# Kernel tuning notes

Measured on AMD Instinct MI355X. Metric: run time of the kernel, lower is better.

## Reference

```python
import jax, jax.numpy as jnp
import numpy as np

T, B, IN_DIM, H = 512, 256, 512, 256  # H == hidden_dim == n_qubits

def setup_inputs() -> dict:
    key = jax.random.key(0)
    ks = jax.random.split(key, 13)
    inputs = jax.random.normal(ks[0], (T, B, IN_DIM), dtype=jnp.float32)
    d = IN_DIM + H
    s = 1.0 / np.sqrt(d)
    def lin(k):
        k1, k2 = jax.random.split(k)
        return (jax.random.uniform(k1, (H, d), jnp.float32, -s, s),
                jax.random.uniform(k2, (H,), jnp.float32, -s, s))
    Wf, bf = lin(ks[1]); Wi, bi = lin(ks[2]); Wg, bg = lin(ks[3]); Wo, bo = lin(ks[4])
    thf = jax.random.uniform(ks[5], (H,), jnp.float32)
    thi = jax.random.uniform(ks[6], (H,), jnp.float32)
    thg = jax.random.uniform(ks[7], (H,), jnp.float32)
    tho = jax.random.uniform(ks[8], (H,), jnp.float32)
    return dict(inputs=inputs, Wf=Wf, bf=bf, thf=thf, Wi=Wi, bi=bi, thi=thi,
                Wg=Wg, bg=bg, thg=thg, Wo=Wo, bo=bo, tho=tho)

def _qgate(combined, W, b, th):
    # Analytic form of the RY+RY+CNOT-ladder circuit with PauliZ expvals:
    # <Z_k> = prod_{i<=k} cos(z_i + theta_i), z = Linear(combined)
    z = combined @ W.T + b  # [B, H]
    return jnp.cumprod(jnp.cos(z + th), axis=-1)

def reference(inputs, Wf, bf, thf, Wi, bi, thi, Wg, bg, thg, Wo, bo, tho):
    batch = inputs.shape[1]
    hx0 = jnp.zeros((batch, H), inputs.dtype)
    cx0 = jnp.zeros((batch, H), inputs.dtype)

    def step(carry, x):
        hx, cx = carry
        comb = jnp.concatenate([x, hx], axis=1)  # [B, IN_DIM+H]
        f = jax.nn.sigmoid(_qgate(comb, Wf, bf, thf))
        i = jax.nn.sigmoid(_qgate(comb, Wi, bi, thi))
        g = jnp.tanh(_qgate(comb, Wg, bg, thg))
        o = jax.nn.sigmoid(_qgate(comb, Wo, bo, tho))
        cx = f * cx + i * g
        hx = o * jnp.tanh(cx)
        return (hx, cx), hx

    (hx, cx), stacked = jax.lax.scan(step, (hx0, cx0), inputs)
    return stacked, hx, cx
```

## Files before the change

kernel.cpp:

```cpp
#include <hip/hip_runtime.h>
#include <hip/hip_bf16.h>
#include <stdint.h>

#define T_STEPS 512
#define BATCH   256
#define HID     256

#define NRWG   128
#define NWWG   128
#define NWG    256
#define RING   4
#define CHUNK  8
#define NCHUNK 64
#define TPC    64
#define SLOT_F (CHUNK*256*1024)

using short8 = __attribute__((ext_vector_type(8))) short;
using f32x4  = __attribute__((ext_vector_type(4))) float;

#define VMCNT0() asm volatile("s_waitcnt vmcnt(0)" ::: "memory")

__device__ inline unsigned short f2bf(float f) {
  unsigned u = __float_as_uint(f);
  unsigned r = (u + 0x7fffu + ((u >> 16) & 1u)) >> 16;
  return (unsigned short)r;
}
__device__ inline float sigm(float x)   { return __builtin_amdgcn_rcpf(1.0f + __expf(-x)); }
__device__ inline float tanh_f(float x) { return 2.0f * __builtin_amdgcn_rcpf(1.0f + __expf(-2.0f * x)) - 1.0f; }

__device__ inline int ld_rlx(const int* p) {
  return __hip_atomic_load(p, __ATOMIC_RELAXED, __HIP_MEMORY_SCOPE_AGENT);
}
__device__ inline void st_rlx(int* p, int v) {
  __hip_atomic_store(p, v, __ATOMIC_RELAXED, __HIP_MEMORY_SCOPE_AGENT);
}
__device__ inline void add_rlx(int* p, int v) {
  __hip_atomic_fetch_add(p, v, __ATOMIC_RELAXED, __HIP_MEMORY_SCOPE_AGENT);
}
__device__ inline float ldg_coh(const float* p) {
  return __hip_atomic_load(p, __ATOMIC_RELAXED, __HIP_MEMORY_SCOPE_AGENT);
}
__device__ inline void stg_coh(float* p, float v) {
  __hip_atomic_store(p, v, __ATOMIC_RELAXED, __HIP_MEMORY_SCOPE_AGENT);
}

__global__ __launch_bounds__(256) void prep_kernel(
    const float* __restrict__ Wf, const float* __restrict__ Wi,
    const float* __restrict__ Wg, const float* __restrict__ Wo,
    const float* __restrict__ bf_, const float* __restrict__ bi_,
    const float* __restrict__ bg_, const float* __restrict__ bo_,
    const float* __restrict__ thf, const float* __restrict__ thi,
    const float* __restrict__ thg, const float* __restrict__ tho,
    unsigned short* __restrict__ Wfull, float* __restrict__ cvec,
    int* __restrict__ flags)
{
  int j = blockIdx.x;
  int g = j >> 8, col = j & 255;
  const float* W  = (g==0)?Wf:(g==1)?Wi:(g==2)?Wg:Wo;
  const float* bb = (g==0)?bf_:(g==1)?bi_:(g==2)?bg_:bo_;
  const float* th = (g==0)?thf:(g==1)?thi:(g==2)?thg:tho;
  const float* wrow = W + (size_t)col * 768;
  for (int k = threadIdx.x; k < 768; k += blockDim.x)
    Wfull[(size_t)j * 768 + k] = f2bf(wrow[k]);
  if (threadIdx.x == 0) cvec[j] = bb[col] + th[col];
  if (j == 0) for (int i = threadIdx.x; i < 512; i += 256) flags[i] = 0;
}

__global__ __launch_bounds__(512, 2) void persist_kernel(
    const float* __restrict__ X,
    const unsigned short* __restrict__ Wfull,
    const float* __restrict__ cvec,
    float* __restrict__ ring,
    float* __restrict__ exch,
    int* __restrict__ done,
    int* __restrict__ consumed,
    int* __restrict__ seq,
    float* __restrict__ out)
{
  __shared__ union {
    struct { unsigned short h[16][264]; float z[8][264]; } rec;
    struct { unsigned short a[128][40]; unsigned short b[256][40]; } gem;
  } sm;

  int bid = blockIdx.x, tid = threadIdx.x;
  int lane = tid & 63, wv = tid >> 6;
  int l15 = lane & 15, lk = lane >> 4;

  if (bid < NRWG) {
    int bg = bid >> 2, g = bid & 3;

    for (int i = tid; i < 16*264; i += 512) ((unsigned short*)sm.rec.h)[i] = 0;

    short8 af[2][8];
#pragma unroll
    for (int ti = 0; ti < 2; ++ti)
#pragma unroll
      for (int kk = 0; kk < 8; ++kk)
        af[ti][kk] = *(const short8*)(Wfull +
            (size_t)(g*256 + wv*32 + ti*16 + l15)*768 + 512 + kk*32 + lk*8);

    float creg[4] = {0.f, 0.f, 0.f, 0.f};
    float zx[4];
    __syncthreads();

    for (int t = 0; t < T_STEPS; ++t) {
      int cIdx = t >> 3;
      if ((t & 7) == 0) {
        if (tid == 0) { while (ld_rlx(&done[cIdx]) < TPC) __builtin_amdgcn_s_sleep(1); }
        __syncthreads();
        const float* zp = ring + (size_t)(cIdx & (RING-1))*SLOT_F
                        + ((size_t)(t & 7)*256 + bg*8 + wv)*1024 + g*256 + lane;
#pragma unroll
        for (int s = 0; s < 4; ++s) zx[s] = ldg_coh(zp + s*64);
      }

      short8 bfr[8];
#pragma unroll
      for (int kk = 0; kk < 8; ++kk)
        bfr[kk] = *(const short8*)&sm.rec.h[l15][kk*32 + lk*8];
      f32x4 acc0 = {0.f,0.f,0.f,0.f}, acc1 = {0.f,0.f,0.f,0.f};
#pragma unroll
      for (int kk = 0; kk < 8; ++kk) {
        acc0 = __builtin_amdgcn_mfma_f32_16x16x32_bf16(af[0][kk], bfr[kk], acc0, 0, 0, 0);
        acc1 = __builtin_amdgcn_mfma_f32_16x16x32_bf16(af[1][kk], bfr[kk], acc1, 0, 0, 0);
      }
      if (l15 < 8) {
        *(f32x4*)&sm.rec.z[l15][wv*32 +      lk*4] = acc0;
        *(f32x4*)&sm.rec.z[l15][wv*32 + 16 + lk*4] = acc1;
      }
      __syncthreads();

      float v[4];
#pragma unroll
      for (int s = 0; s < 4; ++s)
        v[s] = __cosf(sm.rec.z[wv][s*64 + lane] + zx[s]);
#pragma unroll
      for (int off = 1; off < 64; off <<= 1) {
        float u0 = __shfl_up(v[0], (unsigned)off, 64);
        float u1 = __shfl_up(v[1], (unsigned)off, 64);
        float u2 = __shfl_up(v[2], (unsigned)off, 64);
        float u3 = __shfl_up(v[3], (unsigned)off, 64);
        if (lane >= off) { v[0]*=u0; v[1]*=u1; v[2]*=u2; v[3]*=u3; }
      }
      float t0 = __shfl(v[0], 63, 64), t1 = __shfl(v[1], 63, 64), t2 = __shfl(v[2], 63, 64);
      float p1 = t0, p2 = t0*t1, p3 = p2*t2;
      float a0 = v[0], a1 = v[1]*p1, a2 = v[2]*p2, a3 = v[3]*p3;
      float act[4];
      if (g == 2) { act[0]=tanh_f(a0); act[1]=tanh_f(a1); act[2]=tanh_f(a2); act[3]=tanh_f(a3); }
      else        { act[0]=sigm(a0);   act[1]=sigm(a1);   act[2]=sigm(a2);   act[3]=sigm(a3); }

      int par = t & 1;
      float* exw = exch + (((size_t)par*32 + bg)*4 + g)*2048 + wv*256 + lane;
#pragma unroll
      for (int s = 0; s < 4; ++s) stg_coh(exw + s*64, act[s]);
      VMCNT0();
      __syncthreads();
      if (tid == 0) st_rlx(&seq[par*128 + bid], t + 1);

      if (((t+1) & 7) != 0 && t+1 < T_STEPS) {
        const float* zp = ring + (size_t)(((t+1) >> 3) & (RING-1))*SLOT_F
                        + ((size_t)((t+1) & 7)*256 + bg*8 + wv)*1024 + g*256 + lane;
#pragma unroll
        for (int s = 0; s < 4; ++s) zx[s] = ldg_coh(zp + s*64);
      }

      if (lane < 3) {
        int og = (g + 1 + lane) & 3;
        const int* fp = &seq[par*128 + bg*4 + og];
        while (ld_rlx(fp) < t + 1) { }
      }
      asm volatile("" ::: "memory");

      const float* exb = exch + ((size_t)par*32 + bg)*4*2048 + wv*256 + lane;
      float vals[4][4];
#pragma unroll
      for (int q = 0; q < 4; ++q) {
        if (q == g) {
#pragma unroll
          for (int s = 0; s < 4; ++s) vals[q][s] = act[s];
        } else {
#pragma unroll
          for (int s = 0; s < 4; ++s) vals[q][s] = ldg_coh(exb + q*2048 + s*64);
        }
      }

      int brow = bg*8 + wv;
#pragma unroll
      for (int s = 0; s < 4; ++s) {
        float cn = vals[0][s]*creg[s] + vals[1][s]*vals[2][s];
        creg[s] = cn;
        float h = vals[3][s]*tanh_f(cn);
        sm.rec.h[wv][s*64 + lane] = f2bf(h);
        if (g == 0) {
          out[(size_t)t*(BATCH*HID) + (size_t)brow*256 + s*64 + lane] = h;
          if (t == T_STEPS-1) {
            out[(size_t)T_STEPS*(BATCH*HID) + (size_t)brow*256 + s*64 + lane] = h;
            out[(size_t)T_STEPS*(BATCH*HID) + BATCH*HID + (size_t)brow*256 + s*64 + lane] = cn;
          }
        }
      }
      if ((t & 7) == 7 && tid == 0) add_rlx(consumed, 1);
      __syncthreads();
    }
  } else {
    int w0 = bid - NRWG;
    int wr = wv >> 2, wc = wv & 3;
    int rA = tid >> 2, kA = (tid & 3) * 8;
    int rB = tid >> 1, kB = (tid & 1) * 16;

    for (int gt = w0; gt < NCHUNK * TPC; gt += NWWG) {
      int c  = gt >> 6;
      int tl = gt & 63;
      int tm = tl >> 2, tn = tl & 3;

      int need = NRWG * (c - RING + 1);
      if (need > 0) {
        if (tid == 0) { while (ld_rlx(consumed) < need) __builtin_amdgcn_s_sleep(8); }
        __syncthreads();
      }

      const float* Xb = X + ((size_t)c*(CHUNK*256) + (size_t)tm*128) * 512;
      float* slotp = ring + (size_t)(c & (RING-1)) * SLOT_F;

      f32x4 acc[4][4];
#pragma unroll
      for (int mi = 0; mi < 4; ++mi)
#pragma unroll
        for (int ni = 0; ni < 4; ++ni) acc[mi][ni] = (f32x4){0.f,0.f,0.f,0.f};

      for (int kb = 0; kb < 512; kb += 32) {
        const float* ap = Xb + (size_t)rA*512 + kb + kA;
        f32x4 v0 = *(const f32x4*)ap;
        f32x4 v1 = *(const f32x4*)(ap + 4);
        unsigned short t8[8];
        t8[0]=f2bf(v0[0]); t8[1]=f2bf(v0[1]); t8[2]=f2bf(v0[2]); t8[3]=f2bf(v0[3]);
        t8[4]=f2bf(v1[0]); t8[5]=f2bf(v1[1]); t8[6]=f2bf(v1[2]); t8[7]=f2bf(v1[3]);
        *(short8*)&sm.gem.a[rA][kA] = *(short8*)t8;
        const unsigned short* bp = Wfull + (size_t)(tn*256 + rB)*768 + kb + kB;
        *(short8*)&sm.gem.b[rB][kB]     = *(const short8*)bp;
        *(short8*)&sm.gem.b[rB][kB + 8] = *(const short8*)(bp + 8);
        __syncthreads();

        short8 afr[4], bfr4[4];
#pragma unroll
        for (int mi = 0; mi < 4; ++mi) afr[mi]  = *(const short8*)&sm.gem.a[wr*64 + mi*16 + l15][lk*8];
#pragma unroll
        for (int ni = 0; ni < 4; ++ni) bfr4[ni] = *(const short8*)&sm.gem.b[wc*64 + ni*16 + l15][lk*8];
#pragma unroll
        for (int mi = 0; mi < 4; ++mi)
#pragma unroll
          for (int ni = 0; ni < 4; ++ni)
            acc[mi][ni] = __builtin_amdgcn_mfma_f32_16x16x32_bf16(afr[mi], bfr4[ni], acc[mi][ni], 0, 0, 0);
        __syncthreads();
      }

#pragma unroll
      for (int mi = 0; mi < 4; ++mi) {
#pragma unroll
        for (int ni = 0; ni < 4; ++ni) {
          int col = tn*256 + wc*64 + ni*16 + l15;
          float cv = cvec[col];
#pragma unroll
          for (int reg = 0; reg < 4; ++reg) {
            int row = tm*128 + wr*64 + mi*16 + lk*4 + reg;
            stg_coh(&slotp[(size_t)row*1024 + col], acc[mi][ni][reg] + cv);
          }
        }
      }
      VMCNT0();
      __syncthreads();
      if (tid == 0) add_rlx(&done[c], 1);
    }
  }
}

extern "C" void kernel_launch(void* const* d_in, const int* in_sizes, int n_in,
                              void* d_out, int out_size, void* d_ws, size_t ws_size,
                              hipStream_t stream) {
  const float* x   = (const float*)d_in[0];
  const float* Wf  = (const float*)d_in[1];
  const float* bf_ = (const float*)d_in[2];
  const float* thf = (const float*)d_in[3];
  const float* Wi  = (const float*)d_in[4];
  const float* bi_ = (const float*)d_in[5];
  const float* thi = (const float*)d_in[6];
  const float* Wg  = (const float*)d_in[7];
  const float* bg_ = (const float*)d_in[8];
  const float* thg = (const float*)d_in[9];
  const float* Wo  = (const float*)d_in[10];
  const float* bo_ = (const float*)d_in[11];
  const float* tho = (const float*)d_in[12];
  float* out = (float*)d_out;

  char* ws = (char*)d_ws;
  unsigned short* Wfull = (unsigned short*)ws;
  float* cvec  = (float*)(ws + 1572864);
  int*   flags = (int*)(ws + 1576960);
  float* exch  = (float*)(ws + 2097152);
  float* ring  = (float*)(ws + 4194304);

  prep_kernel<<<1024, 256, 0, stream>>>(Wf, Wi, Wg, Wo, bf_, bi_, bg_, bo_,
                                        thf, thi, thg, tho, Wfull, cvec, flags);
  persist_kernel<<<NWG, 512, 0, stream>>>(x, Wfull, cvec, ring, exch,
                                          flags, flags + 128, flags + 256, out);
}
```

Before: 2.209 ms.

## Embed sequence tags in gate exchange packets and swizzle LDS layouts for MFMA

Replaces the per-step exchange of gate activations, which stored data, waited on vmcnt, ran a block barrier and published a separate seq flag, with self-validating 16-byte packets that carry the step number next to the activations. Consumers spin on the packet loads directly, which removes a barrier and a flag round-trip from every timestep of the recurrence. It also prefetches the next chunk's readiness flag so the chunk-boundary wait can be skipped, and moves the recurrent h buffer and the input-GEMM LDS tiles to fragment-ordered, XOR-swizzled layouts so MFMA operand reads avoid bank conflicts. The cost is a larger exchange buffer that must be zeroed in the prep kernel, and correctness now relies on each 16-byte store becoming visible atomically.

```diff
diff --git a/kernel.cpp b/kernel.cpp
--- a/kernel.cpp
+++ b/kernel.cpp
@@ -31,9 +31,6 @@
 __device__ inline int ld_rlx(const int* p) {
   return __hip_atomic_load(p, __ATOMIC_RELAXED, __HIP_MEMORY_SCOPE_AGENT);
 }
-__device__ inline void st_rlx(int* p, int v) {
-  __hip_atomic_store(p, v, __ATOMIC_RELAXED, __HIP_MEMORY_SCOPE_AGENT);
-}
 __device__ inline void add_rlx(int* p, int v) {
   __hip_atomic_fetch_add(p, v, __ATOMIC_RELAXED, __HIP_MEMORY_SCOPE_AGENT);
 }
@@ -43,6 +40,11 @@
 __device__ inline void stg_coh(float* p, float v) {
   __hip_atomic_store(p, v, __ATOMIC_RELAXED, __HIP_MEMORY_SCOPE_AGENT);
 }
+__device__ inline void st16_coh(float* p, f32x4 v) {
+  asm volatile("global_store_dwordx4 %0, %1, off sc0 sc1" :: "v"(p), "v"(v) : "memory");
+}
+
+__device__ inline int hswz(int byte) { return byte ^ (((byte >> 8) & 3) << 4); }
 
 __global__ __launch_bounds__(256) void prep_kernel(
     const float* __restrict__ Wf, const float* __restrict__ Wi,
@@ -52,7 +54,7 @@
     const float* __restrict__ thf, const float* __restrict__ thi,
     const float* __restrict__ thg, const float* __restrict__ tho,
     unsigned short* __restrict__ Wfull, float* __restrict__ cvec,
-    int* __restrict__ flags)
+    int* __restrict__ flags, float* __restrict__ pk)
 {
   int j = blockIdx.x;
   int g = j >> 8, col = j & 255;
@@ -64,6 +66,8 @@
     Wfull[(size_t)j * 768 + k] = f2bf(wrow[k]);
   if (threadIdx.x == 0) cvec[j] = bb[col] + th[col];
   if (j == 0) for (int i = threadIdx.x; i < 512; i += 256) flags[i] = 0;
+  float* pz = pk + (size_t)j * 1024;
+  for (int i = threadIdx.x; i < 1024; i += 256) pz[i] = 0.0f;
 }
 
 __global__ __launch_bounds__(512, 2) void persist_kernel(
@@ -71,15 +75,14 @@
     const unsigned short* __restrict__ Wfull,
     const float* __restrict__ cvec,
     float* __restrict__ ring,
-    float* __restrict__ exch,
+    float* __restrict__ pk,
     int* __restrict__ done,
     int* __restrict__ consumed,
-    int* __restrict__ seq,
     float* __restrict__ out)
 {
   __shared__ union {
-    struct { unsigned short h[16][264]; float z[8][264]; } rec;
-    struct { unsigned short a[128][40]; unsigned short b[256][40]; } gem;
+    struct { unsigned short hL[4096]; float z[8][1032]; int rdy[2]; } rec;
+    struct { unsigned short aL[4096]; unsigned short bL[8192]; } gem;
   } sm;
 
   int bid = blockIdx.x, tid = threadIdx.x;
@@ -89,7 +92,8 @@
   if (bid < NRWG) {
     int bg = bid >> 2, g = bid & 3;
 
-    for (int i = tid; i < 16*264; i += 512) ((unsigned short*)sm.rec.h)[i] = 0;
+    for (int i = tid; i < 4096; i += 512) sm.rec.hL[i] = 0;
+    if (tid == 0) { sm.rec.rdy[0] = 0; sm.rec.rdy[1] = 0; }
 
     short8 af[2][8];
 #pragma unroll
@@ -101,11 +105,12 @@
 
     float creg[4] = {0.f, 0.f, 0.f, 0.f};
     float zx[4];
+    bool pf_prev = false;
     __syncthreads();
 
     for (int t = 0; t < T_STEPS; ++t) {
       int cIdx = t >> 3;
-      if ((t & 7) == 0) {
+      if ((t & 7) == 0 && !pf_prev) {
         if (tid == 0) { while (ld_rlx(&done[cIdx]) < TPC) __builtin_amdgcn_s_sleep(1); }
         __syncthreads();
         const float* zp = ring + (size_t)(cIdx & (RING-1))*SLOT_F
@@ -117,7 +122,7 @@
       short8 bfr[8];
 #pragma unroll
       for (int kk = 0; kk < 8; ++kk)
-        bfr[kk] = *(const short8*)&sm.rec.h[l15][kk*32 + lk*8];
+        bfr[kk] = *(const short8*)((const char*)sm.rec.hL + hswz(kk*1024 + lane*16));
       f32x4 acc0 = {0.f,0.f,0.f,0.f}, acc1 = {0.f,0.f,0.f,0.f};
 #pragma unroll
       for (int kk = 0; kk < 8; ++kk) {
@@ -149,40 +154,57 @@
       if (g == 2) { act[0]=tanh_f(a0); act[1]=tanh_f(a1); act[2]=tanh_f(a2); act[3]=tanh_f(a3); }
       else        { act[0]=sigm(a0);   act[1]=sigm(a1);   act[2]=sigm(a2);   act[3]=sigm(a3); }
 
-      int par = t & 1;
-      float* exw = exch + (((size_t)par*32 + bg)*4 + g)*2048 + wv*256 + lane;
-#pragma unroll
-      for (int s = 0; s < 4; ++s) stg_coh(exw + s*64, act[s]);
-      VMCNT0();
-      __syncthreads();
-      if (tid == 0) st_rlx(&seq[par*128 + bid], t + 1);
-
-      if (((t+1) & 7) != 0 && t+1 < T_STEPS) {
-        const float* zp = ring + (size_t)(((t+1) >> 3) & (RING-1))*SLOT_F
+      int par = t & 1, T1 = t + 1;
+      float seqf = __int_as_float(T1);
+      float* myb = pk + ((((size_t)par*32 + bg)*4 + g)*8 + wv)*512 + (size_t)lane*8;
+      f32x4 P1 = {act[0], act[1], act[2], seqf};
+      f32x4 P2 = {act[3], seqf, 0.f, 0.f};
+      st16_coh(myb, P1);
+      st16_coh(myb + 4, P2);
+
+      int rdyv = sm.rec.rdy[par];
+      bool pf = (((t+1) & 7) == 0) && (t+1 < T_STEPS) && (rdyv >= TPC);
+      if (tid == 0) {
+        int cn = cIdx + 1;
+        sm.rec.rdy[par ^ 1] = ld_rlx(&done[cn]);
+      }
+      if (t+1 < T_STEPS && (((t+1) & 7) != 0 || pf)) {
+        int cN = (t+1) >> 3;
+        const float* zp = ring + (size_t)(cN & (RING-1))*SLOT_F
                         + ((size_t)((t+1) & 7)*256 + bg*8 + wv)*1024 + g*256 + lane;
 #pragma unroll
         for (int s = 0; s < 4; ++s) zx[s] = ldg_coh(zp + s*64);
       }
-
-      if (lane < 3) {
-        int og = (g + 1 + lane) & 3;
-        const int* fp = &seq[par*128 + bg*4 + og];
-        while (ld_rlx(fp) < t + 1) { }
-      }
-      asm volatile("" ::: "memory");
-
-      const float* exb = exch + ((size_t)par*32 + bg)*4*2048 + wv*256 + lane;
+      pf_prev = pf;
+
+      int q0 = (g+1)&3, q1 = (g+2)&3, q2 = (g+3)&3;
+      const float* A1 = pk + ((((size_t)par*32 + bg)*4 + q0)*8 + wv)*512 + (size_t)lane*8;
+      const float* B1 = pk + ((((size_t)par*32 + bg)*4 + q1)*8 + wv)*512 + (size_t)lane*8;
+      const float* C1 = pk + ((((size_t)par*32 + bg)*4 + q2)*8 + wv)*512 + (size_t)lane*8;
+      f32x4 qa1, qa2, qb1, qb2, qc1, qc2;
+      while (true) {
+        asm volatile(
+          "global_load_dwordx4 %0, %6,  off sc0 sc1\n\t"
+          "global_load_dwordx4 %1, %7,  off sc0 sc1\n\t"
+          "global_load_dwordx4 %2, %8,  off sc0 sc1\n\t"
+          "global_load_dwordx4 %3, %9,  off sc0 sc1\n\t"
+          "global_load_dwordx4 %4, %10, off sc0 sc1\n\t"
+          "global_load_dwordx4 %5, %11, off sc0 sc1\n\t"
+          "s_waitcnt vmcnt(0)"
+          : "=&v"(qa1), "=&v"(qa2), "=&v"(qb1), "=&v"(qb2), "=&v"(qc1), "=&v"(qc2)
+          : "v"(A1), "v"(A1+4), "v"(B1), "v"(B1+4), "v"(C1), "v"(C1+4)
+          : "memory");
+        if (__float_as_int(qa1[3]) >= T1 && __float_as_int(qa2[1]) >= T1 &&
+            __float_as_int(qb1[3]) >= T1 && __float_as_int(qb2[1]) >= T1 &&
+            __float_as_int(qc1[3]) >= T1 && __float_as_int(qc2[1]) >= T1) break;
+      }
+
       float vals[4][4];
 #pragma unroll
-      for (int q = 0; q < 4; ++q) {
-        if (q == g) {
-#pragma unroll
-          for (int s = 0; s < 4; ++s) vals[q][s] = act[s];
-        } else {
-#pragma unroll
-          for (int s = 0; s < 4; ++s) vals[q][s] = ldg_coh(exb + q*2048 + s*64);
-        }
-      }
+      for (int s = 0; s < 4; ++s) vals[g][s] = act[s];
+      vals[q0][0]=qa1[0]; vals[q0][1]=qa1[1]; vals[q0][2]=qa1[2]; vals[q0][3]=qa2[0];
+      vals[q1][0]=qb1[0]; vals[q1][1]=qb1[1]; vals[q1][2]=qb1[2]; vals[q1][3]=qb2[0];
+      vals[q2][0]=qc1[0]; vals[q2][1]=qc1[1]; vals[q2][2]=qc1[2]; vals[q2][3]=qc2[0];
 
       int brow = bg*8 + wv;
 #pragma unroll
@@ -190,7 +212,9 @@
         float cn = vals[0][s]*creg[s] + vals[1][s]*vals[2][s];
         creg[s] = cn;
         float h = vals[3][s]*tanh_f(cn);
-        sm.rec.h[wv][s*64 + lane] = f2bf(h);
+        int k = s*64 + lane;
+        int byte = (k >> 5)*1024 + ((((k >> 3) & 3)*16 + wv)*16) + (k & 7)*2;
+        *(unsigned short*)((char*)sm.rec.hL + hswz(byte)) = f2bf(h);
         if (g == 0) {
           out[(size_t)t*(BATCH*HID) + (size_t)brow*256 + s*64 + lane] = h;
           if (t == T_STEPS-1) {
@@ -228,6 +252,12 @@
 #pragma unroll
         for (int ni = 0; ni < 4; ++ni) acc[mi][ni] = (f32x4){0.f,0.f,0.f,0.f};
 
+      int slotA = (rA >> 4)*1024 + ((tid & 3)*16 + (rA & 15))*16;
+      int baseB = (rB >> 4)*1024;
+      int kO = kB >> 3;
+      int slotB0 = baseB + ((kO    )*16 + (rB & 15))*16;
+      int slotB1 = baseB + ((kO + 1)*16 + (rB & 15))*16;
+
       for (int kb = 0; kb < 512; kb += 32) {
         const float* ap = Xb + (size_t)rA*512 + kb + kA;
         f32x4 v0 = *(const f32x4*)ap;
@@ -235,17 +265,19 @@
         unsigned short t8[8];
         t8[0]=f2bf(v0[0]); t8[1]=f2bf(v0[1]); t8[2]=f2bf(v0[2]); t8[3]=f2bf(v0[3]);
         t8[4]=f2bf(v1[0]); t8[5]=f2bf(v1[1]); t8[6]=f2bf(v1[2]); t8[7]=f2bf(v1[3]);
-        *(short8*)&sm.gem.a[rA][kA] = *(short8*)t8;
+        *(short8*)((char*)sm.gem.aL + slotA) = *(short8*)t8;
         const unsigned short* bp = Wfull + (size_t)(tn*256 + rB)*768 + kb + kB;
-        *(short8*)&sm.gem.b[rB][kB]     = *(const short8*)bp;
-        *(short8*)&sm.gem.b[rB][kB + 8] = *(const short8*)(bp + 8);
+        *(short8*)((char*)sm.gem.bL + slotB0) = *(const short8*)bp;
+        *(short8*)((char*)sm.gem.bL + slotB1) = *(const short8*)(bp + 8);
         __syncthreads();
 
         short8 afr[4], bfr4[4];
 #pragma unroll
-        for (int mi = 0; mi < 4; ++mi) afr[mi]  = *(const short8*)&sm.gem.a[wr*64 + mi*16 + l15][lk*8];
-#pragma unroll
-        for (int ni = 0; ni < 4; ++ni) bfr4[ni] = *(const short8*)&sm.gem.b[wc*64 + ni*16 + l15][lk*8];
+        for (int mi = 0; mi < 4; ++mi)
+          afr[mi]  = *(const short8*)((const char*)sm.gem.aL + (wr*4 + mi)*1024 + lane*16);
+#pragma unroll
+        for (int ni = 0; ni < 4; ++ni)
+          bfr4[ni] = *(const short8*)((const char*)sm.gem.bL + (wc*4 + ni)*1024 + lane*16);
 #pragma unroll
         for (int mi = 0; mi < 4; ++mi)
 #pragma unroll
@@ -296,11 +328,11 @@
   unsigned short* Wfull = (unsigned short*)ws;
   float* cvec  = (float*)(ws + 1572864);
   int*   flags = (int*)(ws + 1576960);
-  float* exch  = (float*)(ws + 2097152);
-  float* ring  = (float*)(ws + 4194304);
+  float* pk    = (float*)(ws + 2097152);
+  float* ring  = (float*)(ws + 8388608);
 
   prep_kernel<<<1024, 256, 0, stream>>>(Wf, Wi, Wg, Wo, bf_, bi_, bg_, bo_,
-                                        thf, thi, thg, tho, Wfull, cvec, flags);
-  persist_kernel<<<NWG, 512, 0, stream>>>(x, Wfull, cvec, ring, exch,
-                                          flags, flags + 128, flags + 256, out);
-}
+                                        thf, thi, thg, tho, Wfull, cvec, flags, pk);
+  persist_kernel<<<NWG, 512, 0, stream>>>(x, Wfull, cvec, ring, pk,
+                                          flags, flags + 128, out);
+}
```

Result: slower. 2.623 ms (+18.7%).
